# Performance work log

Measured on AMD Instinct MI355X. Metric: run time of the kernel, lower is better.

The kernel has to match this reference:

```python
import jax, jax.numpy as jnp
import numpy as np

D_MODEL = 256
NHEAD = 8
NLAYERS = 4
B, L, K = 8, 4096, 10
EPS_ATT = 1e-6
EPS_LN = 1e-5
EPS_COS = 1e-8


def setup_inputs() -> dict:
    key = jax.random.key(0)
    ks = jax.random.split(key, 12)
    s = 1.0 / np.sqrt(D_MODEL)
    s2 = 1.0 / np.sqrt(2 * D_MODEL)
    return {
        "ClassNum": K,
        "feat": jax.random.normal(ks[0], (B, L, D_MODEL), jnp.float32),
        "feat_class": jax.random.normal(ks[1], (B, K, D_MODEL), jnp.float32),
        "Wq": jax.random.normal(ks[2], (NLAYERS, D_MODEL, D_MODEL), jnp.float32) * s,
        "Wk": jax.random.normal(ks[3], (NLAYERS, D_MODEL, D_MODEL), jnp.float32) * s,
        "Wv": jax.random.normal(ks[4], (NLAYERS, D_MODEL, D_MODEL), jnp.float32) * s,
        "Wm": jax.random.normal(ks[5], (NLAYERS, D_MODEL, D_MODEL), jnp.float32) * s,
        "W1": jax.random.normal(ks[6], (NLAYERS, 2 * D_MODEL, 2 * D_MODEL), jnp.float32) * s2,
        "W2": jax.random.normal(ks[7], (NLAYERS, 2 * D_MODEL, D_MODEL), jnp.float32) * s2,
        "g1": jnp.ones((NLAYERS, D_MODEL), jnp.float32),
        "b1": jnp.zeros((NLAYERS, D_MODEL), jnp.float32),
        "g2": jnp.ones((NLAYERS, D_MODEL), jnp.float32),
        "b2": jnp.zeros((NLAYERS, D_MODEL), jnp.float32),
    }


def _layernorm(x, g, b):
    mu = jnp.mean(x, axis=-1, keepdims=True)
    xc = x - mu
    var = jnp.mean(xc * xc, axis=-1, keepdims=True)
    return g * xc * jax.lax.rsqrt(var + EPS_LN) + b


def _encoder_layer(x, oh, Wq, Wk, Wv, Wm, W1, W2, g1, b1, g2, b2):
    # x: [B,L,C], oh: [B,L,K] one-hot cluster assignment.
    # Per-cluster LoFTR linear self-attention via segment sums (exact: the
    # per-cluster v_length scaling in LinearAttention cancels algebraically).
    bsz, seq, cdim = x.shape
    hd = cdim // NHEAD
    q = (x @ Wq).reshape(bsz, seq, NHEAD, hd)
    k = (x @ Wk).reshape(bsz, seq, NHEAD, hd)
    v = (x @ Wv).reshape(bsz, seq, NHEAD, hd)
    Q = jax.nn.elu(q) + 1.0
    Kf = jax.nn.elu(k) + 1.0
    # per-(batch,cluster) sums: KV [B,K,H,D,D], Ksum [B,K,H,D]
    KV = jnp.einsum('blc,blhd,blhe->bchde', oh, Kf, v)
    Ksum = jnp.einsum('blc,blhd->bchd', oh, Kf)
    Kt = jnp.einsum('blc,bchd->blhd', oh, Ksum)  # cluster ΣK gathered per token
    Z = 1.0 / (jnp.einsum('blhd,blhd->blh', Q, Kt) + EPS_ATT)
    msg = jnp.zeros((bsz, seq, NHEAD, hd), x.dtype)
    for c in range(oh.shape[-1]):  # small fixed ClassNum loop
        msg = msg + oh[:, :, c][:, :, None, None] * jnp.einsum(
            'blhd,bhde->blhe', Q, KV[:, c])
    msg = msg * Z[..., None]
    m = msg.reshape(bsz, seq, cdim) @ Wm
    m = _layernorm(m, g1, b1)
    h = jnp.concatenate([x, m], axis=-1) @ W1
    h = jax.nn.relu(h) @ W2
    m = _layernorm(h, g2, b2)
    return x + m


def reference(ClassNum, feat, feat_class, Wq, Wk, Wv, Wm, W1, W2, g1, b1, g2, b2):
    x = jax.lax.stop_gradient(feat)          # feat.clone().detach()
    fc = jax.lax.stop_gradient(feat_class)   # feat_class.clone().detach()
    # cosine-similarity top-1 cluster routing (torch.F.cosine_similarity, eps=1e-8)
    na = jnp.linalg.norm(fc, axis=-1)  # [B,K]
    nb = jnp.linalg.norm(x, axis=-1)   # [B,L]
    dot = jnp.einsum('bkc,blc->bkl', fc, x)
    sim = dot / jnp.maximum(na[:, :, None] * nb[:, None, :], EPS_COS)
    seg = jnp.argmax(sim, axis=1)  # [B,L] cluster id per token
    oh = jax.nn.one_hot(seg, ClassNum, dtype=x.dtype)
    for li in range(Wq.shape[0]):
        x = _encoder_layer(x, oh, Wq[li], Wk[li], Wv[li], Wm[li],
                           W1[li], W2[li], g1[li], b1[li], g2[li], b2[li])
    return x
```

## Files before the change

### kernel.cpp

```cpp
#include <hip/hip_runtime.h>
#include <hip/hip_bf16.h>
#include <math.h>

#define DM 256
#define NHEAD 8
#define HD 32
#define NL 4
#define BATCH 8
#define SEQ 4096
#define KCLS 10
#define M_TOK (BATCH*SEQ)

#define BKG 64

#define PADPOS 5120
#define NWIN (PADPOS/64)
#define KVWIN (PADPOS/512)
#define PART_STRIDE (KCLS * 1056)

using bf16x8 = __attribute__((ext_vector_type(8))) short;
using f32x4  = __attribute__((ext_vector_type(4))) float;

__device__ __forceinline__ unsigned short f2bf(float f) {
    __hip_bfloat16 b = __float2bfloat16(f);
    return __builtin_bit_cast(unsigned short, b);
}
__device__ __forceinline__ float bf2f(unsigned short u) {
    unsigned v = (unsigned)u << 16;
    return __builtin_bit_cast(float, v);
}

__device__ __forceinline__ float wave_reduce_sum(float v) {
    #pragma unroll
    for (int off = 32; off > 0; off >>= 1) v += __shfl_xor(v, off, 64);
    return v;
}

__global__ __launch_bounds__(64) void fcn_kernel(const float* __restrict__ fc,
                                                 float* __restrict__ fcn) {
    int bk = blockIdx.x;
    int lane = threadIdx.x;
    float4 fv = *(const float4*)(fc + (size_t)bk * DM + lane * 4);
    float n = fv.x*fv.x + fv.y*fv.y + fv.z*fv.z + fv.w*fv.w;
    n = wave_reduce_sum(n);
    if (lane == 0) fcn[bk] = sqrtf(n);
}

__global__ void route_kernel(const float* __restrict__ feat, const float* __restrict__ fc,
                             const float* __restrict__ fcn,
                             float* __restrict__ x, unsigned short* __restrict__ xm,
                             int* __restrict__ seg) {
    int wid = (int)((blockIdx.x * (size_t)blockDim.x + threadIdx.x) >> 6);
    int lane = threadIdx.x & 63;
    if (wid >= M_TOK) return;
    int b = wid / SEQ;
    float4 xv = *(const float4*)(feat + (size_t)wid * DM + lane * 4);
    *(float4*)(x + (size_t)wid * DM + lane * 4) = xv;
    ushort4 u; u.x = f2bf(xv.x); u.y = f2bf(xv.y); u.z = f2bf(xv.z); u.w = f2bf(xv.w);
    *(ushort4*)(xm + (size_t)wid * 512 + lane * 4) = u;
    float nb2 = xv.x*xv.x + xv.y*xv.y + xv.z*xv.z + xv.w*xv.w;
    nb2 = wave_reduce_sum(nb2);
    float nb = sqrtf(nb2);
    float best = -1e30f; int bestk = 0;
    for (int k = 0; k < KCLS; ++k) {
        float4 fv = *(const float4*)(fc + ((size_t)(b * KCLS + k)) * DM + lane * 4);
        float d = fv.x*xv.x + fv.y*xv.y + fv.z*xv.z + fv.w*xv.w;
        d = wave_reduce_sum(d);
        float sim = d / fmaxf(fcn[b * KCLS + k] * nb, 1e-8f);
        if (sim > best) { best = sim; bestk = k; }
    }
    if (lane == 0) seg[wid] = bestk;
}

__global__ __launch_bounds__(256) void seg_count(const int* __restrict__ seg,
                                                 int* __restrict__ cnt) {
    __shared__ int wc[4][KCLS];
    int b = blockIdx.x >> 4, chunk = blockIdx.x & 15;
    int t = threadIdx.x, w = t >> 6, lane = t & 63;
    int c = seg[b * SEQ + chunk * 256 + t];
    #pragma unroll
    for (int cc = 0; cc < KCLS; ++cc) {
        unsigned long long m = __ballot(c == cc);
        if (lane == 0) wc[w][cc] = __popcll(m);
    }
    __syncthreads();
    if (t < KCLS)
        cnt[(b * 16 + chunk) * KCLS + t] = wc[0][t] + wc[1][t] + wc[2][t] + wc[3][t];
}

__global__ __launch_bounds__(256) void seg_scan(const int* __restrict__ cnt,
                                                int* __restrict__ chunkbase,
                                                int* __restrict__ wseg,
                                                int* __restrict__ psegp) {
    __shared__ int sTot[BATCH][KCLS];
    __shared__ int sBase[BATCH][KCLS];
    int tid = threadIdx.x;
    if (tid < BATCH * KCLS) {
        int b = tid / KCLS, c = tid % KCLS;
        int run = 0;
        #pragma unroll
        for (int j = 0; j < 16; ++j) run += cnt[(b * 16 + j) * KCLS + c];
        sTot[b][c] = run;
    }
    __syncthreads();
    if (tid < BATCH) {
        int b = tid, pb = 0;
        for (int c = 0; c < KCLS; ++c) {
            sBase[b][c] = pb;
            int psz = (sTot[b][c] + 63) & ~63;
            int w0 = pb >> 6, w1 = (pb + psz) >> 6;
            for (int w = w0; w < w1; ++w) wseg[b * NWIN + w] = c;
            pb += psz;
        }
        for (int w = pb >> 6; w < NWIN; ++w) wseg[b * NWIN + w] = -1;
    }
    __syncthreads();
    for (int i = tid; i < BATCH * PADPOS; i += 256) {
        int b = i / PADPOS, pos = i % PADPOS;
        int c = KCLS - 1;
        #pragma unroll
        for (int cc = KCLS - 1; cc >= 1; --cc)
            if (pos < sBase[b][cc]) c = cc - 1;
        psegp[i] = c;
    }
    if (tid < BATCH * KCLS) {
        int b = tid / KCLS, c = tid % KCLS;
        int pre = 0;
        #pragma unroll
        for (int j = 0; j < 16; ++j) {
            chunkbase[(b * 16 + j) * KCLS + c] = sBase[b][c] + pre;
            pre += cnt[(b * 16 + j) * KCLS + c];
        }
    }
}

__global__ __launch_bounds__(256) void seg_scatter(const int* __restrict__ seg,
                                                   const int* __restrict__ chunkbase,
                                                   int* __restrict__ pidxp,
                                                   int* __restrict__ sortposG) {
    __shared__ int wc[4][KCLS];
    int b = blockIdx.x >> 4, chunk = blockIdx.x & 15;
    int t = threadIdx.x, w = t >> 6, lane = t & 63;
    int l = chunk * 256 + t;
    int c = seg[b * SEQ + l];
    int rank_w = 0;
    #pragma unroll
    for (int cc = 0; cc < KCLS; ++cc) {
        unsigned long long m = __ballot(c == cc);
        if (lane == 0) wc[w][cc] = __popcll(m);
        if (cc == c) rank_w = __popcll(m & ((1ULL << lane) - 1ULL));
    }
    __syncthreads();
    int rank = rank_w;
    for (int wp = 0; wp < 4; ++wp)
        if (wp < w) rank += wc[wp][c];
    int pos = chunkbase[(b * 16 + chunk) * KCLS + c] + rank;
    pidxp[b * PADPOS + pos] = l;
    sortposG[b * SEQ + l] = b * PADPOS + pos;
}

__global__ __launch_bounds__(256) void zero_pads(const int* __restrict__ pidxp,
                                                 unsigned short* __restrict__ Kb,
                                                 unsigned short* __restrict__ Vb) {
    int row = blockIdx.x * 8 + (threadIdx.x >> 5);
    int c8 = (threadIdx.x & 31) * 8;
    if (pidxp[row] >= 0) return;
    bf16x8 z = (bf16x8){0,0,0,0,0,0,0,0};
    *(bf16x8*)(Kb + (size_t)row * DM + c8) = z;
    *(bf16x8*)(Vb + (size_t)row * DM + c8) = z;
}

__global__ __launch_bounds__(256) void transpose_bf16(const float* __restrict__ src,
                                                      unsigned short* __restrict__ dst,
                                                      int K, int N) {
    __shared__ float s[64][65];
    int k0 = blockIdx.x * 64, n0 = blockIdx.y * 64;
    int t = threadIdx.x;
    int r = t >> 4, c4 = (t & 15) * 4;
    #pragma unroll
    for (int i = 0; i < 4; ++i) {
        float4 v = *(const float4*)(src + (size_t)(k0 + r + i*16) * N + n0 + c4);
        s[c4+0][r+i*16] = v.x; s[c4+1][r+i*16] = v.y;
        s[c4+2][r+i*16] = v.z; s[c4+3][r+i*16] = v.w;
    }
    __syncthreads();
    #pragma unroll
    for (int i = 0; i < 4; ++i) {
        int nr = r + i*16;
        ushort4 u;
        u.x = f2bf(s[nr][c4+0]); u.y = f2bf(s[nr][c4+1]);
        u.z = f2bf(s[nr][c4+2]); u.w = f2bf(s[nr][c4+3]);
        *(ushort4*)(dst + (size_t)(n0 + nr) * K + k0 + c4) = u;
    }
}

template<int KD, int AS, int MODE>
__global__ __launch_bounds__(512, 4) void mfma_gemm(
    const unsigned short* __restrict__ A, const unsigned short* __restrict__ Bt,
    const int* __restrict__ sortpos,
    unsigned short* __restrict__ Ob0, unsigned short* __restrict__ Ob1,
    unsigned short* __restrict__ Ob2)
{
    __shared__ unsigned short As[128 * BKG];
    __shared__ unsigned short Bs[256 * BKG];
    __shared__ int sPos[128];
    int t = threadIdx.x;
    int lane = t & 63;
    int w = t >> 6;
    int wm = w & 1, wn = w >> 1;
    int bm = blockIdx.x * 128;
    int bn = blockIdx.y * 256;

    if (MODE == 1 && t < 128) sPos[t] = sortpos[bm + t];

    f32x4 acc[4][4];
    #pragma unroll
    for (int m = 0; m < 4; ++m)
        #pragma unroll
        for (int n = 0; n < 4; ++n)
            acc[m][n] = (f32x4){0.f, 0.f, 0.f, 0.f};

    for (int k0 = 0; k0 < KD; k0 += BKG) {
        #pragma unroll
        for (int i = 0; i < 2; ++i) {
            int chunk = i * 512 + t;
            int row = chunk >> 3, cc = chunk & 7;
            __builtin_amdgcn_global_load_lds(
                (const __attribute__((address_space(1))) void*)(A + (size_t)(bm + row) * AS + k0 + cc * 8),
                (__attribute__((address_space(3))) void*)((char*)As + chunk * 16), 16, 0, 0);
        }
        #pragma unroll
        for (int i = 0; i < 4; ++i) {
            int chunk = i * 512 + t;
            int row = chunk >> 3, cc = chunk & 7;
            __builtin_amdgcn_global_load_lds(
                (const __attribute__((address_space(1))) void*)(Bt + (size_t)(bn + row) * KD + k0 + cc * 8),
                (__attribute__((address_space(3))) void*)((char*)Bs + chunk * 16), 16, 0, 0);
        }
        asm volatile("s_waitcnt vmcnt(0)");
        __syncthreads();
        #pragma unroll
        for (int kk = 0; kk < 2; ++kk) {
            int kbyte = (kk * 32 + (lane >> 4) * 8) * 2;
            bf16x8 af[4], bfr[4];
            #pragma unroll
            for (int m = 0; m < 4; ++m)
                af[m] = *(const bf16x8*)((const char*)As + (wm*64 + m*16 + (lane & 15)) * 128 + kbyte);
            #pragma unroll
            for (int n = 0; n < 4; ++n)
                bfr[n] = *(const bf16x8*)((const char*)Bs + (wn*64 + n*16 + (lane & 15)) * 128 + kbyte);
            #pragma unroll
            for (int m = 0; m < 4; ++m)
                #pragma unroll
                for (int n = 0; n < 4; ++n)
                    acc[m][n] = __builtin_amdgcn_mfma_f32_16x16x32_bf16(af[m], bfr[n], acc[m][n], 0, 0, 0);
        }
        __syncthreads();
    }

    int lrow0 = wm * 64 + (lane >> 4) * 4;
    int lcol = wn * 64 + (lane & 15);
    if (MODE == 1) {
        unsigned short* Obuf = (bn < 256) ? Ob0 : (bn < 512) ? Ob1 : Ob2;
        const bool act = (bn < 512);
        #pragma unroll
        for (int m = 0; m < 4; ++m)
            #pragma unroll
            for (int n = 0; n < 4; ++n)
                #pragma unroll
                for (int j = 0; j < 4; ++j) {
                    float v = acc[m][n][j];
                    if (act) v = (v > 0.f) ? v + 1.f : expf(v);
                    int drow = sPos[lrow0 + m*16 + j];
                    Obuf[(size_t)drow * 256 + lcol + n*16] = f2bf(v);
                }
    } else {
        #pragma unroll
        for (int m = 0; m < 4; ++m)
            #pragma unroll
            for (int n = 0; n < 4; ++n)
                #pragma unroll
                for (int j = 0; j < 4; ++j)
                    Ob0[(size_t)(bm + lrow0 + m*16 + j) * 512 + bn + lcol + n*16] =
                        f2bf(fmaxf(acc[m][n][j], 0.f));
    }
}

template<int KD, int LNMODE>
__global__ __launch_bounds__(256) void gemm_ln(
    const unsigned short* __restrict__ A, const unsigned short* __restrict__ Bt,
    const float* __restrict__ g, const float* __restrict__ bb,
    float* __restrict__ x, unsigned short* __restrict__ xm)
{
    __shared__ unsigned short As[64 * BKG];
    __shared__ unsigned short Bs[256 * BKG];
    __shared__ float redS[4][64];
    __shared__ float redQ[4][64];
    int t = threadIdx.x;
    int lane = t & 63;
    int w = t >> 6;
    int li = lane & 15, lg = lane >> 4;
    int bm = blockIdx.x * 64;

    f32x4 acc[4][4];
    #pragma unroll
    for (int m = 0; m < 4; ++m)
        #pragma unroll
        for (int n = 0; n < 4; ++n)
            acc[m][n] = (f32x4){0.f, 0.f, 0.f, 0.f};

    for (int k0 = 0; k0 < KD; k0 += BKG) {
        #pragma unroll
        for (int i = 0; i < 2; ++i) {
            int chunk = i * 256 + t;
            int row = chunk >> 3, cc = chunk & 7;
            __builtin_amdgcn_global_load_lds(
                (const __attribute__((address_space(1))) void*)(A + (size_t)(bm + row) * KD + k0 + cc * 8),
                (__attribute__((address_space(3))) void*)((char*)As + chunk * 16), 16, 0, 0);
        }
        #pragma unroll
        for (int i = 0; i < 8; ++i) {
            int chunk = i * 256 + t;
            int row = chunk >> 3, cc = chunk & 7;
            __builtin_amdgcn_global_load_lds(
                (const __attribute__((address_space(1))) void*)(Bt + (size_t)row * KD + k0 + cc * 8),
                (__attribute__((address_space(3))) void*)((char*)Bs + chunk * 16), 16, 0, 0);
        }
        asm volatile("s_waitcnt vmcnt(0)");
        __syncthreads();
        #pragma unroll
        for (int kk = 0; kk < 2; ++kk) {
            int kbyte = (kk * 32 + lg * 8) * 2;
            bf16x8 af[4], bfr[4];
            #pragma unroll
            for (int m = 0; m < 4; ++m)
                af[m] = *(const bf16x8*)((const char*)As + (m*16 + li) * 128 + kbyte);
            #pragma unroll
            for (int n = 0; n < 4; ++n)
                bfr[n] = *(const bf16x8*)((const char*)Bs + (w*64 + n*16 + li) * 128 + kbyte);
            #pragma unroll
            for (int m = 0; m < 4; ++m)
                #pragma unroll
                for (int n = 0; n < 4; ++n)
                    acc[m][n] = __builtin_amdgcn_mfma_f32_16x16x32_bf16(af[m], bfr[n], acc[m][n], 0, 0, 0);
        }
        __syncthreads();
    }

    float vs[4][4], vq[4][4];
    #pragma unroll
    for (int m = 0; m < 4; ++m)
        #pragma unroll
        for (int j = 0; j < 4; ++j) {
            float s = 0.f, q = 0.f;
            #pragma unroll
            for (int n = 0; n < 4; ++n) {
                float v = acc[m][n][j];
                s += v; q += v * v;
            }
            #pragma unroll
            for (int msk = 1; msk < 16; msk <<= 1) {
                s += __shfl_xor(s, msk, 64);
                q += __shfl_xor(q, msk, 64);
            }
            vs[m][j] = s; vq[m][j] = q;
        }
    if (li == 0) {
        #pragma unroll
        for (int m = 0; m < 4; ++m)
            #pragma unroll
            for (int j = 0; j < 4; ++j) {
                redS[w][m*16 + lg*4 + j] = vs[m][j];
                redQ[w][m*16 + lg*4 + j] = vq[m][j];
            }
    }
    __syncthreads();

    float gv[4], bv[4];
    #pragma unroll
    for (int n = 0; n < 4; ++n) {
        int col = w*64 + n*16 + li;
        gv[n] = g[col]; bv[n] = bb[col];
    }
    #pragma unroll
    for (int m = 0; m < 4; ++m)
        #pragma unroll
        for (int j = 0; j < 4; ++j) {
            int r = m*16 + lg*4 + j;
            float S = redS[0][r] + redS[1][r] + redS[2][r] + redS[3][r];
            float Q = redQ[0][r] + redQ[1][r] + redQ[2][r] + redQ[3][r];
            float mu = S * (1.f / 256.f);
            float var = Q * (1.f / 256.f) - mu * mu;
            float rs = rsqrtf(var + 1e-5f);
            #pragma unroll
            for (int n = 0; n < 4; ++n) {
                int col = w*64 + n*16 + li;
                float o = gv[n] * (acc[m][n][j] - mu) * rs + bv[n];
                if (LNMODE == 1) {
                    xm[(size_t)(bm + r) * 512 + 256 + col] = f2bf(o);
                } else {
                    size_t idx = (size_t)(bm + r) * 256 + col;
                    float xv = x[idx] + o;
                    x[idx] = xv;
                    xm[(size_t)(bm + r) * 512 + col] = f2bf(xv);
                }
            }
        }
}

__global__ __launch_bounds__(256) void kv_kernel(
    const unsigned short* __restrict__ Ksrt, const unsigned short* __restrict__ Vsrt,
    const int* __restrict__ psegp, float* __restrict__ part)
{
    __shared__ unsigned short sK[128 * HD];
    __shared__ unsigned short sV[128 * HD];
    __shared__ int sSeg[8];
    int blk = blockIdx.x;
    int s = blk % KVWIN;
    int bh = blk / KVWIN;
    int b = bh >> 3, h = bh & 7;
    int t = threadIdx.x;
    int d = t >> 3, e0 = (t & 7) * 4;

    if (t < 8) sSeg[t] = psegp[b * PADPOS + s * 512 + t * 64];

    const size_t rowbase = (size_t)(b * PADPOS + s * 512);
    float* pb = part + (size_t)blk * PART_STRIDE;

    float4 a = {0.f, 0.f, 0.f, 0.f};
    float ks = 0.f;
    int ccur = -1;

    for (int chunk = 0; chunk < 4; ++chunk) {
        __syncthreads();
        #pragma unroll
        for (int rep = 0; rep < 2; ++rep) {
            int idx = rep * 256 + t;
            int row = idx >> 2, off8 = (idx & 3) * 8;
            size_t gsrc = (rowbase + chunk * 128 + row) * DM + h * HD + off8;
            *(bf16x8*)(sK + row * HD + off8) = *(const bf16x8*)(Ksrt + gsrc);
            *(bf16x8*)(sV + row * HD + off8) = *(const bf16x8*)(Vsrt + gsrc);
        }
        __syncthreads();

        #pragma unroll
        for (int g = 0; g < 2; ++g) {
            int c = __builtin_amdgcn_readfirstlane(sSeg[chunk * 2 + g]);
            if (c != ccur) {
                if (ccur >= 0) {
                    *(float4*)(pb + ccur * 1056 + d * 32 + e0) = a;
                    if ((t & 7) == 0) pb[ccur * 1056 + 1024 + d] = ks;
                    a = (float4){0.f, 0.f, 0.f, 0.f};
                    ks = 0.f;
                }
                ccur = c;
            }
            #pragma unroll 8
            for (int l = 0; l < 64; ++l) {
                int lr = g * 64 + l;
                float kd = bf2f(sK[lr * HD + d]);
                ushort4 vu = *(const ushort4*)(sV + lr * HD + e0);
                a.x = fmaf(kd, bf2f(vu.x), a.x);
                a.y = fmaf(kd, bf2f(vu.y), a.y);
                a.z = fmaf(kd, bf2f(vu.z), a.z);
                a.w = fmaf(kd, bf2f(vu.w), a.w);
                ks += kd;
            }
        }
    }
    *(float4*)(pb + ccur * 1056 + d * 32 + e0) = a;
    if ((t & 7) == 0) pb[ccur * 1056 + 1024 + d] = ks;
}

__global__ __launch_bounds__(256) void kv_reduce(
    const float* __restrict__ part, const int* __restrict__ psegp,
    float* __restrict__ KV, float* __restrict__ Ks)
{
    int blk = blockIdx.x;
    int c = blk % KCLS;
    int bh = blk / KCLS;
    int b = bh >> 3, h = bh & 7;
    int t = threadIdx.x;
    const float* pb = part + (size_t)bh * KVWIN * PART_STRIDE + c * 1056;
    float4 acc = {0, 0, 0, 0};
    float ka = 0.f;
    #pragma unroll
    for (int s = 0; s < KVWIN; ++s) {
        int cf = psegp[b * PADPOS + s * 512];
        int cl = psegp[b * PADPOS + s * 512 + 511];
        if (c < cf || c > cl) continue;
        float4 v = *(const float4*)(pb + (size_t)s * PART_STRIDE + t * 4);
        acc.x += v.x; acc.y += v.y; acc.z += v.z; acc.w += v.w;
        if (t < 32) ka += pb[(size_t)s * PART_STRIDE + 1024 + t];
    }
    *(float4*)(KV + ((size_t)(b * KCLS + c) * NHEAD + h) * HD * HD + t * 4) = acc;
    if (t < 32) Ks[((size_t)(b * KCLS + c) * NHEAD + h) * HD + t] = ka;
}

__global__ __launch_bounds__(256) void msg_kernel(
    const unsigned short* __restrict__ Qs, const float* __restrict__ KV,
    const float* __restrict__ Ks, const int* __restrict__ pidxp,
    const int* __restrict__ wseg, unsigned short* __restrict__ msgb)
{
    int b = blockIdx.x / NWIN, w = blockIdx.x % NWIN;
    int c = wseg[b * NWIN + w];
    if (c < 0) return;
    __shared__ unsigned short sQ[64 * DM];
    __shared__ unsigned short kvT[NHEAD * HD * HD];
    __shared__ float sKs[NHEAD * HD];
    __shared__ float zl[64 * NHEAD];
    __shared__ int sTok[64];
    int t = threadIdx.x;
    int wv = t >> 6, lane = t & 63;

    if (t < 64) sTok[t] = pidxp[b * PADPOS + w * 64 + t];
    { int h = t >> 5, d = t & 31;
      sKs[h * HD + d] = Ks[((size_t)(b * KCLS + c) * NHEAD + h) * HD + d]; }
    const float* kvsrc = KV + (size_t)(b * KCLS + c) * NHEAD * HD * HD;
    #pragma unroll
    for (int i = 0; i < 8; ++i) {
        int q = i * 256 + t;
        float4 v = ((const float4*)kvsrc)[q];
        int g = q * 4;
        int h = g >> 10, rem = g & 1023;
        int d = rem >> 5, e = rem & 31;
        kvT[h * 1024 + (e + 0) * 32 + d] = f2bf(v.x);
        kvT[h * 1024 + (e + 1) * 32 + d] = f2bf(v.y);
        kvT[h * 1024 + (e + 2) * 32 + d] = f2bf(v.z);
        kvT[h * 1024 + (e + 3) * 32 + d] = f2bf(v.w);
    }
    const unsigned short* qsrc = Qs + (size_t)(b * PADPOS + w * 64) * DM;
    #pragma unroll
    for (int i = 0; i < 8; ++i) {
        int q = i * 256 + t;
        *(bf16x8*)(sQ + q * 8) = *(const bf16x8*)(qsrc + q * 8);
    }
    __syncthreads();

    #pragma unroll
    for (int i = 0; i < 2; ++i) {
        int idx = i * 256 + t;
        int r = idx >> 3, h = idx & 7;
        float z = 0.f;
        #pragma unroll
        for (int d8 = 0; d8 < 4; ++d8) {
            bf16x8 qv = *(const bf16x8*)(sQ + r * DM + h * 32 + d8 * 8);
            #pragma unroll
            for (int j = 0; j < 8; ++j)
                z = fmaf(bf2f((unsigned short)qv[j]), sKs[h * HD + d8 * 8 + j], z);
        }
        zl[r * NHEAD + h] = z;
    }
    __syncthreads();

    int li = lane & 15, lg = lane >> 4;
    #pragma unroll
    for (int hh = 0; hh < 2; ++hh) {
        int h = wv * 2 + hh;
        f32x4 acc[4][2];
        #pragma unroll
        for (int m = 0; m < 4; ++m)
            #pragma unroll
            for (int n = 0; n < 2; ++n)
                acc[m][n] = (f32x4){0.f, 0.f, 0.f, 0.f};
        bf16x8 bfr[2];
        #pragma unroll
        for (int n = 0; n < 2; ++n)
            bfr[n] = *(const bf16x8*)(kvT + h * 1024 + (n * 16 + li) * 32 + lg * 8);
        #pragma unroll
        for (int m = 0; m < 4; ++m) {
            bf16x8 af = *(const bf16x8*)(sQ + (m * 16 + li) * DM + h * 32 + lg * 8);
            #pragma unroll
            for (int n = 0; n < 2; ++n)
                acc[m][n] = __builtin_amdgcn_mfma_f32_16x16x32_bf16(af, bfr[n], acc[m][n], 0, 0, 0);
        }
        #pragma unroll
        for (int m = 0; m < 4; ++m)
            #pragma unroll
            for (int n = 0; n < 2; ++n)
                #pragma unroll
                for (int j = 0; j < 4; ++j) {
                    int r = m * 16 + lg * 4 + j;
                    int tok = sTok[r];
                    if (tok >= 0) {
                        float o = acc[m][n][j] / (zl[r * NHEAD + h] + 1e-6f);
                        msgb[(size_t)(b * SEQ + tok) * DM + h * 32 + n * 16 + li] = f2bf(o);
                    }
                }
    }
}

extern "C" void kernel_launch(void* const* d_in, const int* in_sizes, int n_in,
                              void* d_out, int out_size, void* d_ws, size_t ws_size,
                              hipStream_t stream)
{
    const float* feat = (const float*)d_in[1];
    const float* fc   = (const float*)d_in[2];
    const float* Wq   = (const float*)d_in[3];
    const float* Wk   = (const float*)d_in[4];
    const float* Wv   = (const float*)d_in[5];
    const float* Wm   = (const float*)d_in[6];
    const float* W1   = (const float*)d_in[7];
    const float* W2   = (const float*)d_in[8];
    const float* g1   = (const float*)d_in[9];
    const float* b1   = (const float*)d_in[10];
    const float* g2   = (const float*)d_in[11];
    const float* b2   = (const float*)d_in[12];
    float* x = (float*)d_out;

    char* ws = (char*)d_ws;
    auto alloc = [&](size_t bytes) { char* p = ws; ws += (bytes + 255) & ~(size_t)255; return p; };
    int*   seg    = (int*)  alloc((size_t)M_TOK * 4);
    int*   cnt    = (int*)  alloc((size_t)BATCH * 16 * KCLS * 4);
    int*   cbase  = (int*)  alloc((size_t)BATCH * 16 * KCLS * 4);
    int*   pidxp  = (int*)  alloc((size_t)BATCH * PADPOS * 4);
    int*   psegp  = (int*)  alloc((size_t)BATCH * PADPOS * 4);
    int*   sortposG = (int*)alloc((size_t)M_TOK * 4);
    int*   wseg   = (int*)  alloc((size_t)BATCH * NWIN * 4);
    float* fcn    = (float*)alloc((size_t)BATCH * KCLS * 4);
    float* KV     = (float*)alloc((size_t)BATCH * KCLS * NHEAD * HD * HD * 4);
    float* Ks     = (float*)alloc((size_t)BATCH * KCLS * NHEAD * HD * 4);
    unsigned short* xm = (unsigned short*)alloc((size_t)M_TOK * 512 * 2);
    char* bufA = alloc((size_t)M_TOK * 512 * 2);
    unsigned short* Qs   = (unsigned short*)alloc((size_t)BATCH * PADPOS * DM * 2);
    unsigned short* Ksrt = (unsigned short*)alloc((size_t)BATCH * PADPOS * DM * 2);
    unsigned short* Vsrt = (unsigned short*)alloc((size_t)BATCH * PADPOS * DM * 2);
    unsigned short* WqkvT = (unsigned short*)alloc((size_t)NL * 768 * 256 * 2);
    unsigned short* WmT   = (unsigned short*)alloc((size_t)NL * 256 * 256 * 2);
    unsigned short* W1T   = (unsigned short*)alloc((size_t)NL * 512 * 512 * 2);
    unsigned short* W2T   = (unsigned short*)alloc((size_t)NL * 256 * 512 * 2);

    unsigned short* hb   = (unsigned short*)bufA;
    unsigned short* msgb = (unsigned short*)bufA;
    float*          part = (float*)bufA;

    for (int li = 0; li < NL; ++li) {
        transpose_bf16<<<dim3(4, 4), 256, 0, stream>>>(Wq + (size_t)li*65536, WqkvT + (size_t)li*768*256, 256, 256);
        transpose_bf16<<<dim3(4, 4), 256, 0, stream>>>(Wk + (size_t)li*65536, WqkvT + (size_t)li*768*256 + 65536, 256, 256);
        transpose_bf16<<<dim3(4, 4), 256, 0, stream>>>(Wv + (size_t)li*65536, WqkvT + (size_t)li*768*256 + 131072, 256, 256);
        transpose_bf16<<<dim3(4, 4), 256, 0, stream>>>(Wm + (size_t)li*65536, WmT + (size_t)li*65536, 256, 256);
        transpose_bf16<<<dim3(8, 8), 256, 0, stream>>>(W1 + (size_t)li*262144, W1T + (size_t)li*262144, 512, 512);
        transpose_bf16<<<dim3(8, 4), 256, 0, stream>>>(W2 + (size_t)li*131072, W2T + (size_t)li*131072, 512, 256);
    }

    fcn_kernel<<<BATCH * KCLS, 64, 0, stream>>>(fc, fcn);
    route_kernel<<<8192, 256, 0, stream>>>(feat, fc, fcn, x, xm, seg);

    seg_count<<<BATCH * 16, 256, 0, stream>>>(seg, cnt);
    seg_scan<<<1, 256, 0, stream>>>(cnt, cbase, wseg, psegp);
    hipMemsetAsync(pidxp, 0xFF, (size_t)BATCH * PADPOS * 4, stream);
    seg_scatter<<<BATCH * 16, 256, 0, stream>>>(seg, cbase, pidxp, sortposG);
    zero_pads<<<BATCH * PADPOS / 8, 256, 0, stream>>>(pidxp, Ksrt, Vsrt);

    for (int li = 0; li < NL; ++li) {
        const unsigned short* wqkv = WqkvT + (size_t)li * 768 * 256;
        const unsigned short* wm   = WmT + (size_t)li * 65536;
        const unsigned short* w1   = W1T + (size_t)li * 262144;
        const unsigned short* w2   = W2T + (size_t)li * 131072;

        mfma_gemm<256, 512, 1><<<dim3(256, 3), 512, 0, stream>>>(xm, wqkv, sortposG, Qs, Ksrt, Vsrt);

        kv_kernel<<<BATCH * NHEAD * KVWIN, 256, 0, stream>>>(Ksrt, Vsrt, psegp, part);
        kv_reduce<<<BATCH * NHEAD * KCLS, 256, 0, stream>>>(part, psegp, KV, Ks);

        msg_kernel<<<BATCH * NWIN, 256, 0, stream>>>(Qs, KV, Ks, pidxp, wseg, msgb);

        gemm_ln<256, 1><<<512, 256, 0, stream>>>(msgb, wm, g1 + li * DM, b1 + li * DM, nullptr, xm);

        mfma_gemm<512, 512, 2><<<dim3(256, 2), 512, 0, stream>>>(xm, w1, nullptr, hb, nullptr, nullptr);

        gemm_ln<512, 2><<<512, 256, 0, stream>>>(hb, w2, g2 + li * DM, b2 + li * DM, x, xm);
    }
}
```

Measured before the change: 781.9 us.

## Restructure KV partials to per-64-row groups with fp32 padded shared tiles

The KV accumulation kernel now handles 256-row windows (twice as many blocks) and writes one partial per 64-row group instead of per-class partials, dropping the segment tracking. K/V are converted to fp32 when staged and stored in padded shared arrays so the inner loop reads conflict-free floats without per-element bf16 conversion. The reduce kernel then sums the 80 group partials whose class matches, which costs more partial traffic and more loop iterations per reduce block.

```diff
diff --git a/kernel.cpp b/kernel.cpp
--- a/kernel.cpp
+++ b/kernel.cpp
@@ -15,8 +15,8 @@
 
 #define PADPOS 5120
 #define NWIN (PADPOS/64)
-#define KVWIN (PADPOS/512)
-#define PART_STRIDE (KCLS * 1056)
+#define KVWIN 20
+#define NGRP (KVWIN*4)
 
 using bf16x8 = __attribute__((ext_vector_type(8))) short;
 using f32x4  = __attribute__((ext_vector_type(4))) float;
@@ -410,66 +410,56 @@
 
 __global__ __launch_bounds__(256) void kv_kernel(
     const unsigned short* __restrict__ Ksrt, const unsigned short* __restrict__ Vsrt,
-    const int* __restrict__ psegp, float* __restrict__ part)
+    float* __restrict__ part)
 {
-    __shared__ unsigned short sK[128 * HD];
-    __shared__ unsigned short sV[128 * HD];
-    __shared__ int sSeg[8];
+    __shared__ float sK[64 * 33];
+    __shared__ float sV[64 * 33];
     int blk = blockIdx.x;
     int s = blk % KVWIN;
     int bh = blk / KVWIN;
     int b = bh >> 3, h = bh & 7;
     int t = threadIdx.x;
     int d = t >> 3, e0 = (t & 7) * 4;
-
-    if (t < 8) sSeg[t] = psegp[b * PADPOS + s * 512 + t * 64];
-
-    const size_t rowbase = (size_t)(b * PADPOS + s * 512);
-    float* pb = part + (size_t)blk * PART_STRIDE;
-
-    float4 a = {0.f, 0.f, 0.f, 0.f};
-    float ks = 0.f;
-    int ccur = -1;
-
-    for (int chunk = 0; chunk < 4; ++chunk) {
+    int srow = t >> 2, soff = (t & 3) * 8;
+    const size_t rowbase = (size_t)(b * PADPOS + s * 256);
+    float* pball = part + ((size_t)bh * NGRP + s * 4) * 1056;
+
+    for (int g = 0; g < 4; ++g) {
+        size_t gsrc = (rowbase + g * 64 + srow) * DM + h * HD + soff;
+        bf16x8 k8 = *(const bf16x8*)(Ksrt + gsrc);
+        bf16x8 v8 = *(const bf16x8*)(Vsrt + gsrc);
+        float4 ka, kb, va, vb;
+        ka.x = bf2f((unsigned short)k8[0]); ka.y = bf2f((unsigned short)k8[1]);
+        ka.z = bf2f((unsigned short)k8[2]); ka.w = bf2f((unsigned short)k8[3]);
+        kb.x = bf2f((unsigned short)k8[4]); kb.y = bf2f((unsigned short)k8[5]);
+        kb.z = bf2f((unsigned short)k8[6]); kb.w = bf2f((unsigned short)k8[7]);
+        va.x = bf2f((unsigned short)v8[0]); va.y = bf2f((unsigned short)v8[1]);
+        va.z = bf2f((unsigned short)v8[2]); va.w = bf2f((unsigned short)v8[3]);
+        vb.x = bf2f((unsigned short)v8[4]); vb.y = bf2f((unsigned short)v8[5]);
+        vb.z = bf2f((unsigned short)v8[6]); vb.w = bf2f((unsigned short)v8[7]);
+        *(float4*)(sK + srow * 33 + soff)     = ka;
+        *(float4*)(sK + srow * 33 + soff + 4) = kb;
+        *(float4*)(sV + srow * 33 + soff)     = va;
+        *(float4*)(sV + srow * 33 + soff + 4) = vb;
         __syncthreads();
-        #pragma unroll
-        for (int rep = 0; rep < 2; ++rep) {
-            int idx = rep * 256 + t;
-            int row = idx >> 2, off8 = (idx & 3) * 8;
-            size_t gsrc = (rowbase + chunk * 128 + row) * DM + h * HD + off8;
-            *(bf16x8*)(sK + row * HD + off8) = *(const bf16x8*)(Ksrt + gsrc);
-            *(bf16x8*)(sV + row * HD + off8) = *(const bf16x8*)(Vsrt + gsrc);
-        }
+
+        float4 a = {0.f, 0.f, 0.f, 0.f};
+        float ks = 0.f;
+        #pragma unroll 8
+        for (int l = 0; l < 64; ++l) {
+            float kd = sK[l * 33 + d];
+            float4 v4 = *(const float4*)(sV + l * 33 + e0);
+            a.x = fmaf(kd, v4.x, a.x);
+            a.y = fmaf(kd, v4.y, a.y);
+            a.z = fmaf(kd, v4.z, a.z);
+            a.w = fmaf(kd, v4.w, a.w);
+            ks += kd;
+        }
+        float* pb = pball + g * 1056;
+        *(float4*)(pb + d * 32 + e0) = a;
+        if ((t & 7) == 0) pb[1024 + d] = ks;
         __syncthreads();
-
-        #pragma unroll
-        for (int g = 0; g < 2; ++g) {
-            int c = __builtin_amdgcn_readfirstlane(sSeg[chunk * 2 + g]);
-            if (c != ccur) {
-                if (ccur >= 0) {
-                    *(float4*)(pb + ccur * 1056 + d * 32 + e0) = a;
-                    if ((t & 7) == 0) pb[ccur * 1056 + 1024 + d] = ks;
-                    a = (float4){0.f, 0.f, 0.f, 0.f};
-                    ks = 0.f;
-                }
-                ccur = c;
-            }
-            #pragma unroll 8
-            for (int l = 0; l < 64; ++l) {
-                int lr = g * 64 + l;
-                float kd = bf2f(sK[lr * HD + d]);
-                ushort4 vu = *(const ushort4*)(sV + lr * HD + e0);
-                a.x = fmaf(kd, bf2f(vu.x), a.x);
-                a.y = fmaf(kd, bf2f(vu.y), a.y);
-                a.z = fmaf(kd, bf2f(vu.z), a.z);
-                a.w = fmaf(kd, bf2f(vu.w), a.w);
-                ks += kd;
-            }
-        }
-    }
-    *(float4*)(pb + ccur * 1056 + d * 32 + e0) = a;
-    if ((t & 7) == 0) pb[ccur * 1056 + 1024 + d] = ks;
+    }
 }
 
 __global__ __launch_bounds__(256) void kv_reduce(
@@ -481,17 +471,15 @@
     int bh = blk / KCLS;
     int b = bh >> 3, h = bh & 7;
     int t = threadIdx.x;
-    const float* pb = part + (size_t)bh * KVWIN * PART_STRIDE + c * 1056;
+    const float* pb = part + (size_t)bh * NGRP * 1056;
     float4 acc = {0, 0, 0, 0};
     float ka = 0.f;
-    #pragma unroll
-    for (int s = 0; s < KVWIN; ++s) {
-        int cf = psegp[b * PADPOS + s * 512];
-        int cl = psegp[b * PADPOS + s * 512 + 511];
-        if (c < cf || c > cl) continue;
-        float4 v = *(const float4*)(pb + (size_t)s * PART_STRIDE + t * 4);
+    for (int gg = 0; gg < NGRP; ++gg) {
+        int cg = psegp[b * PADPOS + gg * 64];
+        if (cg != c) continue;
+        float4 v = *(const float4*)(pb + (size_t)gg * 1056 + t * 4);
         acc.x += v.x; acc.y += v.y; acc.z += v.z; acc.w += v.w;
-        if (t < 32) ka += pb[(size_t)s * PART_STRIDE + 1024 + t];
+        if (t < 32) ka += pb[(size_t)gg * 1056 + 1024 + t];
     }
     *(float4*)(KV + ((size_t)(b * KCLS + c) * NHEAD + h) * HD * HD + t * 4) = acc;
     if (t < 32) Ks[((size_t)(b * KCLS + c) * NHEAD + h) * HD + t] = ka;
@@ -660,7 +648,7 @@
 
         mfma_gemm<256, 512, 1><<<dim3(256, 3), 512, 0, stream>>>(xm, wqkv, sortposG, Qs, Ksrt, Vsrt);
 
-        kv_kernel<<<BATCH * NHEAD * KVWIN, 256, 0, stream>>>(Ksrt, Vsrt, psegp, part);
+        kv_kernel<<<BATCH * NHEAD * KVWIN, 256, 0, stream>>>(Ksrt, Vsrt, part);
         kv_reduce<<<BATCH * NHEAD * KCLS, 256, 0, stream>>>(part, psegp, KV, Ks);
 
         msg_kernel<<<BATCH * NWIN, 256, 0, stream>>>(Qs, KV, Ks, pidxp, wseg, msgb);
```

Measured after the change: 812.6 us. 3.9% more time.
